# Kernel tuning notes

Hardware: AMD Instinct MI355X
Metric: run time of the kernel (lower is better)

The kernel has to match this reference:

```python
import jax, jax.numpy as jnp
import numpy as np
from jax import lax

DX = 1.0
DT = 0.01
NT = 1000  # T / dt = 10 / 0.01


def setup_inputs() -> dict:
    key = jax.random.key(0)
    u0 = jax.random.uniform(key, (64, 2048), dtype=jnp.float32)
    return {
        "u0": u0,
        "c": jnp.float32(1.0),
        "alpha": jnp.float32(1.0),
        "beta": jnp.float32(1.0),
    }


def reference(u0, c, alpha, beta):
    """Explicit-Euler finite-difference KS solver with periodic BCs:
        u_t = -c * u * u_x - alpha * u_xx - beta * u_xxxx
    Returns the full trajectory stacked over time: (NT+1, B, N)."""
    inv_2dx = 1.0 / (2.0 * DX)
    inv_dx2 = 1.0 / (DX * DX)
    inv_dx4 = 1.0 / (DX ** 4)

    def step(u, _):
        up1 = jnp.roll(u, -1, axis=-1)
        um1 = jnp.roll(u, 1, axis=-1)
        up2 = jnp.roll(u, -2, axis=-1)
        um2 = jnp.roll(u, 2, axis=-1)
        u_x = (up1 - um1) * inv_2dx
        u_xx = (up1 - 2.0 * u + um1) * inv_dx2
        u_xxxx = (up2 - 4.0 * up1 + 6.0 * u - 4.0 * um1 + um2) * inv_dx4
        u_new = u + DT * (-c * u * u_x - alpha * u_xx - beta * u_xxxx)
        return u_new, u_new

    _, traj = lax.scan(step, u0, None, length=NT)
    return jnp.concatenate([u0[None], traj], axis=0)  # (NT+1, B, N)
```

## Files before the change

kernel.cpp:

```cpp
#include <hip/hip_runtime.h>

#define NCOL  2048
#define NROW  64
#define NSTEP 1000
#define NTH   256
#define EPT   8
#define NSEG  4
#define SEGLEN (NSTEP / NSEG)

typedef float vf4 __attribute__((ext_vector_type(4)));
typedef float vf2 __attribute__((ext_vector_type(2)));

__global__ __launch_bounds__(NTH) void ks_kernel(
    const float* __restrict__ u0,
    const float* __restrict__ c_in,
    const float* __restrict__ alpha_in,
    const float* __restrict__ beta_in,
    float* __restrict__ out)
{
    __shared__ vf2 xch[2][2][NTH];

    const int bid = blockIdx.x;
    const int row = bid & (NROW - 1);
    const int seg = bid >> 6;
    const int tid = threadIdx.x;

    const float c     = c_in[0];
    const float alpha = alpha_in[0];
    const float beta  = beta_in[0];

    const float dt     = 0.01f;
    const float inv2dx = 0.5f;
    const float invdx2 = 1.0f;
    const float invdx4 = 1.0f;

    const float* __restrict__ urow = u0 + (size_t)row * NCOL;
    vf4 a = ((const vf4*)urow)[tid * 2 + 0];
    vf4 b = ((const vf4*)urow)[tid * 2 + 1];
    float u[EPT] = {a.x, a.y, a.z, a.w, b.x, b.y, b.z, b.w};

    if (seg == 0) {
        float* orow0 = out + (size_t)row * NCOL + tid * EPT;
        __builtin_nontemporal_store(a, (vf4*)orow0);
        __builtin_nontemporal_store(b, (vf4*)orow0 + 1);
    }

    int p = 0;
    auto step = [&]() {
        vf2 lo = {u[0], u[1]};
        vf2 hi = {u[6], u[7]};
        xch[p][0][tid] = lo;
        xch[p][1][tid] = hi;
        asm volatile("s_waitcnt lgkmcnt(0)\n\ts_barrier" ::: "memory");
        vf2 L = xch[p][1][(tid - 1) & (NTH - 1)];
        vf2 R = xch[p][0][(tid + 1) & (NTH - 1)];

        float w[12];
        w[0] = L.x; w[1] = L.y;
        #pragma unroll
        for (int i = 0; i < EPT; ++i) w[2 + i] = u[i];
        w[10] = R.x; w[11] = R.y;

        constexpr int ord[EPT] = {2, 3, 4, 5, 0, 1, 6, 7};
        #pragma unroll
        for (int k = 0; k < EPT; ++k) {
            const int i = ord[k];
            float um2 = w[i];
            float um1 = w[i + 1];
            float uc  = w[i + 2];
            float up1 = w[i + 3];
            float up2 = w[i + 4];
            float u_x    = (up1 - um1) * inv2dx;
            float u_xx   = (up1 - 2.0f * uc + um1) * invdx2;
            float u_xxxx = (up2 - 4.0f * up1 + 6.0f * uc - 4.0f * um1 + um2) * invdx4;
            u[i] = uc + dt * (-c * uc * u_x - alpha * u_xx - beta * u_xxxx);
        }
        p ^= 1;
    };

    const int warm = seg * SEGLEN;
    for (int t = 0; t < warm; ++t) step();

    const size_t slab = (size_t)NROW * NCOL;
    float* outp = out + (size_t)(warm + 1) * slab + (size_t)row * NCOL + tid * EPT;
    for (int t = 0; t < SEGLEN; ++t) {
        step();
        vf4 na = {u[0], u[1], u[2], u[3]};
        vf4 nb = {u[4], u[5], u[6], u[7]};
        __builtin_nontemporal_store(na, (vf4*)outp);
        __builtin_nontemporal_store(nb, (vf4*)outp + 1);
        outp += slab;
    }
}

extern "C" void kernel_launch(void* const* d_in, const int* in_sizes, int n_in,
                              void* d_out, int out_size, void* d_ws, size_t ws_size,
                              hipStream_t stream) {
    const float* u0    = (const float*)d_in[0];
    const float* c     = (const float*)d_in[1];
    const float* alpha = (const float*)d_in[2];
    const float* beta  = (const float*)d_in[3];
    float* out = (float*)d_out;

    ks_kernel<<<NROW * NSEG, NTH, 0, stream>>>(u0, c, alpha, beta, out);
}
```

Measured before the change: 742.8 us.

## Use wide halos to take four time steps per barrier exchange

Each thread now exchanges an 8-element halo on each side through shared memory and then advances four time steps locally with redundant overlap computation, so there is one barrier per four steps instead of one per step. The four blocks per row no longer split the trajectory into time segments with warm-up. Each block recomputes the whole trajectory and stores only the step whose index modulo four matches its group, which removes the warm-up imbalance between segments. In exchange, each thread does more arithmetic in the overlapping halo region and holds more registers.

```diff
diff --git a/kernel.cpp b/kernel.cpp
--- a/kernel.cpp
+++ b/kernel.cpp
@@ -5,25 +5,50 @@
 #define NSTEP 1000
 #define NTH   256
 #define EPT   8
-#define NSEG  4
-#define SEGLEN (NSTEP / NSEG)
+#define S     4
+#define HALO  (2*S)
+#define WIN   (EPT + 2*HALO)
+#define NSPLIT 4
 
 typedef float vf4 __attribute__((ext_vector_type(4)));
-typedef float vf2 __attribute__((ext_vector_type(2)));
 
-__global__ __launch_bounds__(NTH) void ks_kernel(
+
+#define DOSTEP(dst, src, LO, HI) do {                                         \
+    _Pragma("unroll")                                                         \
+    for (int k = (LO); k < (HI); ++k) {                                       \
+        float um2 = (src)[k-2];                                               \
+        float um1 = (src)[k-1];                                               \
+        float uc  = (src)[k];                                                 \
+        float up1 = (src)[k+1];                                               \
+        float up2 = (src)[k+2];                                               \
+        float u_x    = (up1 - um1) * inv2dx;                                  \
+        float u_xx   = (up1 - 2.0f * uc + um1) * invdx2;                      \
+        float u_xxxx = (up2 - 4.0f * up1 + 6.0f * uc - 4.0f * um1 + um2) * invdx4; \
+        (dst)[k] = uc + dt * (-c * uc * u_x - alpha * u_xx - beta * u_xxxx);  \
+    }                                                                         \
+} while (0)
+
+#define STORE8(arr) do {                                                      \
+    vf4 sa = { (arr)[8],  (arr)[9],  (arr)[10], (arr)[11] };                  \
+    vf4 sb = { (arr)[12], (arr)[13], (arr)[14], (arr)[15] };                  \
+    __builtin_nontemporal_store(sa, (vf4*)outp);                              \
+    __builtin_nontemporal_store(sb, (vf4*)outp + 1);                          \
+} while (0)
+
+__global__ __launch_bounds__(NTH, 1) void ks_kernel(
     const float* __restrict__ u0,
     const float* __restrict__ c_in,
     const float* __restrict__ alpha_in,
     const float* __restrict__ beta_in,
     float* __restrict__ out)
 {
-    __shared__ vf2 xch[2][2][NTH];
+    __shared__ float xbuf[2][NCOL];
 
     const int bid = blockIdx.x;
     const int row = bid & (NROW - 1);
-    const int seg = bid >> 6;
+    const int g   = bid >> 6;
     const int tid = threadIdx.x;
+    const int base = tid * EPT;
 
     const float c     = c_in[0];
     const float alpha = alpha_in[0];
@@ -34,62 +59,50 @@
     const float invdx2 = 1.0f;
     const float invdx4 = 1.0f;
 
+    float W[WIN], V[WIN];
+
     const float* __restrict__ urow = u0 + (size_t)row * NCOL;
-    vf4 a = ((const vf4*)urow)[tid * 2 + 0];
-    vf4 b = ((const vf4*)urow)[tid * 2 + 1];
-    float u[EPT] = {a.x, a.y, a.z, a.w, b.x, b.y, b.z, b.w};
+    vf4 a  = ((const vf4*)urow)[tid * 2 + 0];
+    vf4 b2 = ((const vf4*)urow)[tid * 2 + 1];
+    W[8]  = a.x;  W[9]  = a.y;  W[10] = a.z;  W[11] = a.w;
+    W[12] = b2.x; W[13] = b2.y; W[14] = b2.z; W[15] = b2.w;
 
-    if (seg == 0) {
-        float* orow0 = out + (size_t)row * NCOL + tid * EPT;
-        __builtin_nontemporal_store(a, (vf4*)orow0);
-        __builtin_nontemporal_store(b, (vf4*)orow0 + 1);
+    if (g == 0) {
+        float* orow0 = out + (size_t)row * NCOL + base;
+        __builtin_nontemporal_store(a,  (vf4*)orow0);
+        __builtin_nontemporal_store(b2, (vf4*)orow0 + 1);
     }
 
+    const size_t slab = (size_t)NROW * NCOL;
+    float* outp = out + (size_t)(g + 1) * slab + (size_t)row * NCOL + base;
+
     int p = 0;
-    auto step = [&]() {
-        vf2 lo = {u[0], u[1]};
-        vf2 hi = {u[6], u[7]};
-        xch[p][0][tid] = lo;
-        xch[p][1][tid] = hi;
+    for (int bq = 0; bq < NSTEP / S; ++bq) {
+        vf4 wa = { W[8],  W[9],  W[10], W[11] };
+        vf4 wb = { W[12], W[13], W[14], W[15] };
+        *(vf4*)&xbuf[p][base]     = wa;
+        *(vf4*)&xbuf[p][base + 4] = wb;
         asm volatile("s_waitcnt lgkmcnt(0)\n\ts_barrier" ::: "memory");
-        vf2 L = xch[p][1][(tid - 1) & (NTH - 1)];
-        vf2 R = xch[p][0][(tid + 1) & (NTH - 1)];
+        vf4 l0 = *(const vf4*)&xbuf[p][(base - 8)  & (NCOL - 1)];
+        vf4 l1 = *(const vf4*)&xbuf[p][(base - 4)  & (NCOL - 1)];
+        vf4 r0 = *(const vf4*)&xbuf[p][(base + 8)  & (NCOL - 1)];
+        vf4 r1 = *(const vf4*)&xbuf[p][(base + 12) & (NCOL - 1)];
+        W[0]  = l0.x; W[1]  = l0.y; W[2]  = l0.z; W[3]  = l0.w;
+        W[4]  = l1.x; W[5]  = l1.y; W[6]  = l1.z; W[7]  = l1.w;
+        W[16] = r0.x; W[17] = r0.y; W[18] = r0.z; W[19] = r0.w;
+        W[20] = r1.x; W[21] = r1.y; W[22] = r1.z; W[23] = r1.w;
+        p ^= 1;
 
-        float w[12];
-        w[0] = L.x; w[1] = L.y;
-        #pragma unroll
-        for (int i = 0; i < EPT; ++i) w[2 + i] = u[i];
-        w[10] = R.x; w[11] = R.y;
+        DOSTEP(V, W, 2, 22);
+        if (g == 0) STORE8(V);
+        DOSTEP(W, V, 4, 20);
+        if (g == 1) STORE8(W);
+        DOSTEP(V, W, 6, 18);
+        if (g == 2) STORE8(V);
+        DOSTEP(W, V, 8, 16);
+        if (g == 3) STORE8(W);
 
-        constexpr int ord[EPT] = {2, 3, 4, 5, 0, 1, 6, 7};
-        #pragma unroll
-        for (int k = 0; k < EPT; ++k) {
-            const int i = ord[k];
-            float um2 = w[i];
-            float um1 = w[i + 1];
-            float uc  = w[i + 2];
-            float up1 = w[i + 3];
-            float up2 = w[i + 4];
-            float u_x    = (up1 - um1) * inv2dx;
-            float u_xx   = (up1 - 2.0f * uc + um1) * invdx2;
-            float u_xxxx = (up2 - 4.0f * up1 + 6.0f * uc - 4.0f * um1 + um2) * invdx4;
-            u[i] = uc + dt * (-c * uc * u_x - alpha * u_xx - beta * u_xxxx);
-        }
-        p ^= 1;
-    };
-
-    const int warm = seg * SEGLEN;
-    for (int t = 0; t < warm; ++t) step();
-
-    const size_t slab = (size_t)NROW * NCOL;
-    float* outp = out + (size_t)(warm + 1) * slab + (size_t)row * NCOL + tid * EPT;
-    for (int t = 0; t < SEGLEN; ++t) {
-        step();
-        vf4 na = {u[0], u[1], u[2], u[3]};
-        vf4 nb = {u[4], u[5], u[6], u[7]};
-        __builtin_nontemporal_store(na, (vf4*)outp);
-        __builtin_nontemporal_store(nb, (vf4*)outp + 1);
-        outp += slab;
+        outp += (size_t)S * slab;
     }
 }
 
@@ -102,5 +115,5 @@
     const float* beta  = (const float*)d_in[3];
     float* out = (float*)d_out;
 
-    ks_kernel<<<NROW * NSEG, NTH, 0, stream>>>(u0, c, alpha, beta, out);
+    ks_kernel<<<NROW * NSPLIT, NTH, 0, stream>>>(u0, c, alpha, beta, out);
 }
```

After: 732.6 us. Within noise of the previous version (-1.4%).
